# Optimization experiments

Hardware: AMD Instinct MI355X
Metric: run time of the kernel (lower is better)

The kernel has to match this reference:

```python
import jax, jax.numpy as jnp
import numpy as np

D_MODEL = 512
NUM_HEADS = 8
HEAD_DIM = D_MODEL // NUM_HEADS
WINDOW = 64


def setup_inputs() -> dict:
    key = jax.random.key(0)
    ks = jax.random.split(key, 9)
    B, S = 2, 4096
    s = 1.0 / np.sqrt(D_MODEL)
    x = jax.random.normal(ks[0], (B, S, D_MODEL), dtype=jnp.float32)
    Wq = jax.random.uniform(ks[1], (D_MODEL, D_MODEL), jnp.float32, -s, s)
    bq = jax.random.uniform(ks[2], (D_MODEL,), jnp.float32, -s, s)
    Wk = jax.random.uniform(ks[3], (D_MODEL, D_MODEL), jnp.float32, -s, s)
    bk = jax.random.uniform(ks[4], (D_MODEL,), jnp.float32, -s, s)
    Wv = jax.random.uniform(ks[5], (D_MODEL, D_MODEL), jnp.float32, -s, s)
    bv = jax.random.uniform(ks[6], (D_MODEL,), jnp.float32, -s, s)
    Wo = jax.random.uniform(ks[7], (D_MODEL, D_MODEL), jnp.float32, -s, s)
    bo = jax.random.uniform(ks[8], (D_MODEL,), jnp.float32, -s, s)
    return {"x": x, "Wq": Wq, "bq": bq, "Wk": Wk, "bk": bk,
            "Wv": Wv, "bv": bv, "Wo": Wo, "bo": bo}


def reference(x, Wq, bq, Wk, bk, Wv, bv, Wo, bo):
    B, S, _ = x.shape
    # projections (torch Linear: x @ W.T + b)
    q = (x @ Wq.T + bq).reshape(B, S, NUM_HEADS, HEAD_DIM).transpose(0, 2, 1, 3)
    k = (x @ Wk.T + bk).reshape(B, S, NUM_HEADS, HEAD_DIM).transpose(0, 2, 1, 3)
    v = (x @ Wv.T + bv).reshape(B, S, NUM_HEADS, HEAD_DIM).transpose(0, 2, 1, 3)
    scores = jnp.einsum('bhqd,bhkd->bhqk', q, k) / jnp.sqrt(
        jnp.asarray(HEAD_DIM, x.dtype))
    idx = jnp.arange(S)
    local = jnp.abs(idx[None, :] - idx[:, None]) <= WINDOW  # [S,S]
    scores = jnp.where(local[None, None], scores, -jnp.inf)
    attn = jax.nn.softmax(scores, axis=-1)
    out = jnp.einsum('bhqk,bhkd->bhqd', attn, v)
    out = out.transpose(0, 2, 1, 3).reshape(B, S, D_MODEL)
    return out @ Wo.T + bo
```

## Files before the change

kernel.cpp:

```cpp
#include <hip/hip_runtime.h>
#include <hip/hip_bf16.h>

typedef __attribute__((ext_vector_type(8))) short short8;
typedef __attribute__((ext_vector_type(4))) short s16x4;
typedef __attribute__((ext_vector_type(4))) float f32x4;

#define S_LEN 4096
#define DM 512
#define NH 8
#define HD 64
#define NB 2

__device__ __forceinline__ ushort f2bf(float f) {
    union { float f; unsigned int i; } x; x.f = f;
    unsigned int i = x.i;
    unsigned int r = (i + 0x7fffu + ((i >> 16) & 1u)) >> 16;
    return (ushort)r;
}

__device__ __forceinline__ void gload16(const ushort* g, ushort* l) {
    __builtin_amdgcn_global_load_lds(
        (const __attribute__((address_space(1))) unsigned int*)(g),
        (__attribute__((address_space(3))) unsigned int*)(l),
        16, 0, 0);
}

__device__ __forceinline__ f32x4 mfma16(s16x4 a, s16x4 b, f32x4 c) {
#if __has_builtin(__builtin_amdgcn_mfma_f32_16x16x16bf16_1k)
    return __builtin_amdgcn_mfma_f32_16x16x16bf16_1k(a, b, c, 0, 0, 0);
#else
    f32x4 d;
    asm volatile("v_mfma_f32_16x16x16_bf16 %0, %1, %2, %3"
                 : "=v"(d) : "v"(a), "v"(b), "v"(c));
    return d;
#endif
}

__global__ __launch_bounds__(256) void cvt_all_kernel(
    const float* __restrict__ x,
    const float* __restrict__ s0, const float* __restrict__ s1,
    const float* __restrict__ s2, const float* __restrict__ s3,
    ushort* __restrict__ xb,
    ushort* __restrict__ t0, ushort* __restrict__ t1,
    ushort* __restrict__ t2, ushort* __restrict__ t3)
{
    const float* src;
    ushort* dst;
    size_t i;
    if (blockIdx.x < 2048) {
        src = x; dst = xb;
        i = (size_t)blockIdx.x * 256 + threadIdx.x;
    } else {
        const int wb = blockIdx.x - 2048;
        const int which = wb >> 7;
        src = (which == 0) ? s0 : (which == 1) ? s1 : (which == 2) ? s2 : s3;
        dst = (which == 0) ? t0 : (which == 1) ? t1 : (which == 2) ? t2 : t3;
        i = (size_t)(wb & 127) * 256 + threadIdx.x;
    }
    const float4* s = (const float4*)src;
    float4 a = s[i * 2], b = s[i * 2 + 1];
    short8 o;
    o[0] = (short)f2bf(a.x); o[1] = (short)f2bf(a.y);
    o[2] = (short)f2bf(a.z); o[3] = (short)f2bf(a.w);
    o[4] = (short)f2bf(b.x); o[5] = (short)f2bf(b.y);
    o[6] = (short)f2bf(b.z); o[7] = (short)f2bf(b.w);
    *(short8*)(dst + i * 8) = o;
}

__global__ __launch_bounds__(256) void qkv_proj_kernel(
    const ushort* __restrict__ X,
    const ushort* __restrict__ Wq, const float* __restrict__ bq,
    const ushort* __restrict__ Wk, const float* __restrict__ bk,
    const ushort* __restrict__ Wv, const float* __restrict__ bv,
    ushort* __restrict__ Qws, ushort* __restrict__ Kws, ushort* __restrict__ Vt)
{
    __shared__ __align__(1024) ushort As[128 * 64];
    __shared__ __align__(1024) ushort Bs[3][64 * 64];

    const int lane = threadIdx.x & 63;
    const int w    = threadIdx.x >> 6;
    const int xcd  = blockIdx.x & 7;
    const int idx  = blockIdx.x >> 3;
    const int tc   = idx & 7;
    const int tr   = xcd + 8 * (idx >> 3);
    const int c0   = tc * 64;
    const int r0   = tr * 128;

    const ushort* Wm[3] = { Wq, Wk, Wv };
    const float*  bm[3] = { bq, bk, bv };

    const int lr = lane & 15;
    const int lg = lane >> 4;
    const int ldrow = lane >> 3;
    const int ldcol = (lane & 7) * 8;

    f32x4 acc[3][2][4] = {};
    for (int ks = 0; ks < 8; ks++) {
        const int k0 = ks * 64;
        if (ks) __syncthreads();
        const ushort* gA = X + (size_t)(r0 + ldrow) * DM + k0 + ldcol;
#pragma unroll
        for (int j = 0; j < 4; j++) {
            const int ch = w * 4 + j;
            gload16(gA + (size_t)ch * 8 * DM, As + ch * 512);
        }
#pragma unroll
        for (int j = 0; j < 6; j++) {
            const int q = w * 6 + j;
            const int mat = q >> 3, ch = q & 7;
            gload16(Wm[mat] + (size_t)(c0 + ch * 8 + ldrow) * DM + k0 + ldcol,
                    &Bs[mat][ch * 512]);
        }
        __syncthreads();

#pragma unroll
        for (int kk = 0; kk < 2; kk++) {
            const int koff = kk * 32 + lg * 8;
            short8 a[2], b[3][4];
#pragma unroll
            for (int m = 0; m < 2; m++)
                a[m] = *(const short8*)(As + (w * 32 + 16 * m + lr) * 64 + koff);
#pragma unroll
            for (int mat = 0; mat < 3; mat++)
#pragma unroll
                for (int n = 0; n < 4; n++)
                    b[mat][n] = *(const short8*)(&Bs[mat][(16 * n + lr) * 64 + koff]);
#pragma unroll
            for (int mat = 0; mat < 3; mat++)
#pragma unroll
                for (int m = 0; m < 2; m++)
#pragma unroll
                    for (int n = 0; n < 4; n++)
                        acc[mat][m][n] = __builtin_amdgcn_mfma_f32_16x16x32_bf16(
                            a[m], b[mat][n], acc[mat][m][n], 0, 0, 0);
        }
    }

#pragma unroll
    for (int mat = 0; mat < 3; mat++) {
#pragma unroll
        for (int n = 0; n < 4; n++) {
            const int c = c0 + 16 * n + lr;
            const float bb = bm[mat][c];
            const int h = c >> 6, d = c & 63;
#pragma unroll
            for (int m = 0; m < 2; m++) {
                const int row0 = r0 + w * 32 + 16 * m + 4 * lg;
                const int bidx = row0 >> 12;
                const int s0 = row0 & (S_LEN - 1);
                if (mat == 2) {
                    uint2 u;
                    u.x = (uint)f2bf(acc[2][m][n][0] + bb) |
                          ((uint)f2bf(acc[2][m][n][1] + bb) << 16);
                    u.y = (uint)f2bf(acc[2][m][n][2] + bb) |
                          ((uint)f2bf(acc[2][m][n][3] + bb) << 16);
                    *(uint2*)(Vt + ((size_t)(bidx * NH + h) * HD + d) * S_LEN + s0) = u;
                } else {
                    ushort* dst = (mat == 0) ? Qws : Kws;
#pragma unroll
                    for (int r = 0; r < 4; r++)
                        dst[((size_t)(bidx * NH + h) * S_LEN + s0 + r) * HD + d] =
                            f2bf(acc[mat][m][n][r] + bb);
                }
            }
        }
    }
}

__global__ __launch_bounds__(256) void attn_kernel(
    const ushort* __restrict__ Qws, const ushort* __restrict__ Kws,
    const ushort* __restrict__ Vt, ushort* __restrict__ AO)
{
    __shared__ __align__(1024) ushort Ks[192 * 64];
    __shared__ __align__(1024) ushort Vs[64 * 192];

    const int x   = blockIdx.x;
    const int xcd = x & 7;
    const int idx = x >> 3;
    const int bh  = xcd * 2 + (idx >> 6);
    const int qb  = idx & 63;
    const int w   = threadIdx.x >> 6;
    const int lane = threadIdx.x & 63;
    const int lr = lane & 15;
    const int lg = lane >> 4;

    const ushort* Qh = Qws + (size_t)bh * S_LEN * HD;
    const ushort* Kh = Kws + (size_t)bh * S_LEN * HD;
    const ushort* Vh = Vt  + (size_t)bh * HD * S_LEN;

    const int q0 = qb * 64 + w * 16;
    const int kstart = qb * 64 - 64;

#pragma unroll
    for (int i = 0; i < 6; i++) {
        const int sb = w * 384 + i * 64;
        const int s = sb + lane;
        const int row = s >> 3;
        const int g = (s & 7) ^ (row & 7);
        int rg = kstart + row;
        rg = (rg < 0) ? 0 : (rg >= S_LEN ? S_LEN - 1 : rg);
        gload16(Kh + (size_t)rg * HD + g * 8, Ks + sb * 8);
    }
#pragma unroll
    for (int i = 0; i < 6; i++) {
        const int sb = w * 384 + i * 64;
        const int s = sb + lane;
        const int row = s / 24;
        const int sr = s - row * 24;
        const int cr = sr ^ (row & 7);
        int cg = kstart + cr * 8;
        cg = (cg < 0) ? 0 : (cg > S_LEN - 8 ? S_LEN - 8 : cg);
        gload16(Vh + (size_t)row * S_LEN + cg, Vs + sb * 8);
    }

    short8 qa[2];
#pragma unroll
    for (int kk = 0; kk < 2; kk++)
        qa[kk] = *(const short8*)(Qh + (size_t)(q0 + lr) * HD + kk * 32 + lg * 8);

    __syncthreads();

    const int swz = (lr & 7) << 3;

    f32x4 sc[12];
#pragma unroll
    for (int ct = 0; ct < 12; ct++) {
        sc[ct] = f32x4{0.f, 0.f, 0.f, 0.f};
        const int base = (ct * 16 + lr) * 64;
        short8 kb0 = *(const short8*)(Ks + (base + ((0  + lg * 8) ^ swz)));
        short8 kb1 = *(const short8*)(Ks + (base + ((32 + lg * 8) ^ swz)));
        sc[ct] = __builtin_amdgcn_mfma_f32_16x16x32_bf16(kb0, qa[0], sc[ct], 0, 0, 0);
        sc[ct] = __builtin_amdgcn_mfma_f32_16x16x32_bf16(kb1, qa[1], sc[ct], 0, 0, 0);
    }

    const float scale2 = 0.18033688f;
    const int qi = q0 + lr;
    float sum = 0.f;
#pragma unroll
    for (int ct = 0; ct < 12; ct++) {
#pragma unroll
        for (int r = 0; r < 4; r++) {
            const int j = kstart + ct * 16 + 4 * lg + r;
            const bool valid = (j >= 0) && (j < S_LEN) && (qi - j <= 64) && (j - qi <= 64);
            const float p = valid ? exp2f(sc[ct][r] * scale2) : 0.f;
            sc[ct][r] = p;
            sum += p;
        }
    }
    sum += __shfl_xor(sum, 16);
    sum += __shfl_xor(sum, 32);
    const float inv = 1.0f / sum;

    s16x4 pb[12];
#pragma unroll
    for (int ct = 0; ct < 12; ct++) {
        pb[ct][0] = (short)f2bf(sc[ct][0]);
        pb[ct][1] = (short)f2bf(sc[ct][1]);
        pb[ct][2] = (short)f2bf(sc[ct][2]);
        pb[ct][3] = (short)f2bf(sc[ct][3]);
    }

    f32x4 po[4] = {};
#pragma unroll
    for (int ct = 0; ct < 12; ct++) {
        const int k0 = ct * 16 + 4 * lg;
        const int sub = k0 & 7;
        const int ch = k0 >> 3;
#pragma unroll
        for (int n = 0; n < 4; n++) {
            const int d = 16 * n + lr;
            s16x4 va = *(const s16x4*)(Vs + d * 192 + 8 * (ch ^ (lr & 7)) + sub);
            po[n] = mfma16(va, pb[ct], po[n]);
        }
    }

    const int b = bh >> 3, h = bh & 7;
    ushort* aorow = AO + ((size_t)(b * S_LEN + q0 + lr)) * DM + h * HD;
#pragma unroll
    for (int n = 0; n < 4; n++) {
        uint2 u;
        u.x = (uint)f2bf(po[n][0] * inv) | ((uint)f2bf(po[n][1] * inv) << 16);
        u.y = (uint)f2bf(po[n][2] * inv) | ((uint)f2bf(po[n][3] * inv) << 16);
        *(uint2*)(aorow + 16 * n + 4 * lg) = u;
    }
}

__global__ __launch_bounds__(256) void out_proj_kernel(
    const ushort* __restrict__ AO, const ushort* __restrict__ Wo,
    const float* __restrict__ bo, float* __restrict__ Out)
{
    __shared__ __align__(1024) ushort As[64 * 64];
    __shared__ __align__(1024) ushort Bs[128 * 64];

    const int lane = threadIdx.x & 63;
    const int w    = threadIdx.x >> 6;
    const int xcd  = blockIdx.x & 7;
    const int idx  = blockIdx.x >> 3;
    const int tr   = xcd + 8 * (idx >> 2);
    const int tc   = idx & 3;
    const int c0   = tc * 128;
    const int r0   = tr * 64;
    const int lr = lane & 15;
    const int lg = lane >> 4;
    const int wr = w >> 1, wc = w & 1;
    const int ldrow = lane >> 3;
    const int ldcol = (lane & 7) * 8;

    f32x4 acc[2][4] = {};
    for (int ks = 0; ks < 8; ks++) {
        const int k0 = ks * 64;
        if (ks) __syncthreads();
        const ushort* gA = AO + (size_t)(r0 + ldrow) * DM + k0 + ldcol;
        const ushort* gB = Wo + (size_t)(c0 + ldrow) * DM + k0 + ldcol;
#pragma unroll
        for (int j = 0; j < 2; j++) {
            const int ch = w * 2 + j;
            gload16(gA + (size_t)ch * 8 * DM, As + ch * 512);
        }
#pragma unroll
        for (int j = 0; j < 4; j++) {
            const int ch = w * 4 + j;
            gload16(gB + (size_t)ch * 8 * DM, Bs + ch * 512);
        }
        __syncthreads();

#pragma unroll
        for (int kk = 0; kk < 2; kk++) {
            const int koff = kk * 32 + lg * 8;
            short8 a[2], b[4];
#pragma unroll
            for (int m = 0; m < 2; m++)
                a[m] = *(const short8*)(As + (wr * 32 + 16 * m + lr) * 64 + koff);
#pragma unroll
            for (int n = 0; n < 4; n++)
                b[n] = *(const short8*)(Bs + (wc * 64 + 16 * n + lr) * 64 + koff);
#pragma unroll
            for (int m = 0; m < 2; m++)
#pragma unroll
                for (int n = 0; n < 4; n++)
                    acc[m][n] = __builtin_amdgcn_mfma_f32_16x16x32_bf16(a[m], b[n], acc[m][n], 0, 0, 0);
        }
    }

#pragma unroll
    for (int n = 0; n < 4; n++) {
        const int c = c0 + wc * 64 + 16 * n + lr;
        const float bb = bo[c];
#pragma unroll
        for (int m = 0; m < 2; m++) {
#pragma unroll
            for (int r = 0; r < 4; r++) {
                const int row = r0 + wr * 32 + 16 * m + 4 * lg + r;
                Out[(size_t)row * DM + c] = acc[m][n][r] + bb;
            }
        }
    }
}

extern "C" void kernel_launch(void* const* d_in, const int* in_sizes, int n_in,
                              void* d_out, int out_size, void* d_ws, size_t ws_size,
                              hipStream_t stream) {
    const float* x  = (const float*)d_in[0];
    const float* Wq = (const float*)d_in[1];
    const float* bq = (const float*)d_in[2];
    const float* Wk = (const float*)d_in[3];
    const float* bk = (const float*)d_in[4];
    const float* Wv = (const float*)d_in[5];
    const float* bv = (const float*)d_in[6];
    const float* Wo = (const float*)d_in[7];
    const float* bo = (const float*)d_in[8];
    float* out = (float*)d_out;

    const size_t XE = (size_t)NB * S_LEN * DM;
    const size_t WE = (size_t)DM * DM;

    ushort* Xb  = (ushort*)d_ws;
    ushort* Wqb = Xb + XE;
    ushort* Wkb = Wqb + WE;
    ushort* Wvb = Wkb + WE;
    ushort* Wob = Wvb + WE;
    ushort* Qws = Wob + WE;
    ushort* Kws = Qws + XE;
    ushort* Vt  = Kws + XE;
    ushort* AO  = Vt + XE;

    cvt_all_kernel<<<2560, 256, 0, stream>>>(x, Wq, Wk, Wv, Wo, Xb, Wqb, Wkb, Wvb, Wob);
    qkv_proj_kernel<<<512, 256, 0, stream>>>(Xb, Wqb, bq, Wkb, bk, Wvb, bv, Qws, Kws, Vt);
    attn_kernel<<<1024, 256, 0, stream>>>(Qws, Kws, Vt, AO);
    out_proj_kernel<<<512, 256, 0, stream>>>(AO, Wob, bo, out);
}
```

Before: 58.29 us.

## Fuse all four stages into one persistent cooperative kernel with grid syncs

Adds a persistent cooperative kernel that runs conversion, QKV projection, windowed attention and output projection in sequence, separated by grid-wide syncs and using grid-stride loops over virtual blocks. It is launched through hipLaunchCooperativeKernel when supported, capped at 512 blocks, and falls back to the four separate launches otherwise. The aim is to remove per-kernel launch overhead and inter-kernel gaps. In exchange it accepts grid.sync costs, a smaller grid than the separate kernels used, and extra host-side attribute and occupancy queries on every call.

```diff
diff --git a/kernel.cpp b/kernel.cpp
--- a/kernel.cpp
+++ b/kernel.cpp
@@ -1,5 +1,8 @@
 #include <hip/hip_runtime.h>
 #include <hip/hip_bf16.h>
+#include <hip/hip_cooperative_groups.h>
+
+namespace cg = cooperative_groups;
 
 typedef __attribute__((ext_vector_type(8))) short short8;
 typedef __attribute__((ext_vector_type(4))) short s16x4;
@@ -34,6 +37,317 @@
                  : "=v"(d) : "v"(a), "v"(b), "v"(c));
     return d;
 #endif
+}
+
+__global__ __launch_bounds__(256) void fused_kernel(
+    const float* __restrict__ x,
+    const float* __restrict__ Wq, const float* __restrict__ bq,
+    const float* __restrict__ Wk, const float* __restrict__ bk,
+    const float* __restrict__ Wv, const float* __restrict__ bv,
+    const float* __restrict__ Wo, const float* __restrict__ bo,
+    float* __restrict__ Out,
+    ushort* __restrict__ Xb, ushort* __restrict__ Wqb, ushort* __restrict__ Wkb,
+    ushort* __restrict__ Wvb, ushort* __restrict__ Wob,
+    ushort* __restrict__ Qws, ushort* __restrict__ Kws,
+    ushort* __restrict__ Vtp, ushort* __restrict__ AO)
+{
+    __shared__ __align__(1024) ushort lds[16384];
+
+    cg::grid_group grid = cg::this_grid();
+
+    const int lane = threadIdx.x & 63;
+    const int w    = threadIdx.x >> 6;
+    const int lr = lane & 15;
+    const int lg = lane >> 4;
+    const int ldrow = lane >> 3;
+    const int ldcol = (lane & 7) * 8;
+
+    {
+        const int stride = gridDim.x * 256;
+        const int tid = blockIdx.x * 256 + threadIdx.x;
+        for (int t = tid; t < 655360; t += stride) {
+            const float* src; ushort* dst; size_t i;
+            if (t < 524288) { src = x; dst = Xb; i = (size_t)t; }
+            else {
+                const int wt = t - 524288;
+                const int which = wt >> 15;
+                i = (size_t)(wt & 32767);
+                src = (which == 0) ? Wq : (which == 1) ? Wk : (which == 2) ? Wv : Wo;
+                dst = (which == 0) ? Wqb : (which == 1) ? Wkb : (which == 2) ? Wvb : Wob;
+            }
+            const float4* s = (const float4*)src;
+            float4 a = s[i * 2], b = s[i * 2 + 1];
+            short8 o;
+            o[0] = (short)f2bf(a.x); o[1] = (short)f2bf(a.y);
+            o[2] = (short)f2bf(a.z); o[3] = (short)f2bf(a.w);
+            o[4] = (short)f2bf(b.x); o[5] = (short)f2bf(b.y);
+            o[6] = (short)f2bf(b.z); o[7] = (short)f2bf(b.w);
+            *(short8*)(dst + i * 8) = o;
+        }
+    }
+    grid.sync();
+
+    {
+        ushort* As  = lds;
+        ushort* Bsp = lds + 4096;
+        const ushort* Wm[3] = { Wqb, Wkb, Wvb };
+        const float*  bm[3] = { bq, bk, bv };
+
+        for (int vb = blockIdx.x; vb < 1024; vb += gridDim.x) {
+            __syncthreads();
+            const int xcd = vb & 7;
+            const int idx = vb >> 3;
+            const int tc  = idx & 7;
+            const int tr  = xcd + 8 * (idx >> 3);
+            const int c0  = tc * 64;
+            const int r0  = tr * 64;
+
+            f32x4 acc[3][4] = {};
+            for (int ks = 0; ks < 8; ks++) {
+                const int k0 = ks * 64;
+                if (ks) __syncthreads();
+                const ushort* gA = Xb + (size_t)(r0 + ldrow) * DM + k0 + ldcol;
+#pragma unroll
+                for (int j = 0; j < 2; j++) {
+                    const int ch = w * 2 + j;
+                    gload16(gA + (size_t)ch * 8 * DM, As + ch * 512);
+                }
+#pragma unroll
+                for (int j = 0; j < 6; j++) {
+                    const int q = w * 6 + j;
+                    const int mat = q >> 3, ch = q & 7;
+                    gload16(Wm[mat] + (size_t)(c0 + ch * 8 + ldrow) * DM + k0 + ldcol,
+                            Bsp + mat * 4096 + ch * 512);
+                }
+                __syncthreads();
+
+#pragma unroll
+                for (int kk = 0; kk < 2; kk++) {
+                    const int koff = kk * 32 + lg * 8;
+                    short8 a = *(const short8*)(As + (w * 16 + lr) * 64 + koff);
+#pragma unroll
+                    for (int mat = 0; mat < 3; mat++)
+#pragma unroll
+                        for (int n = 0; n < 4; n++) {
+                            short8 b = *(const short8*)(Bsp + mat * 4096 + (16 * n + lr) * 64 + koff);
+                            acc[mat][n] = __builtin_amdgcn_mfma_f32_16x16x32_bf16(
+                                a, b, acc[mat][n], 0, 0, 0);
+                        }
+                }
+            }
+
+#pragma unroll
+            for (int mat = 0; mat < 3; mat++) {
+#pragma unroll
+                for (int n = 0; n < 4; n++) {
+                    const int c = c0 + 16 * n + lr;
+                    const float bb = bm[mat][c];
+                    const int h = c >> 6, d = c & 63;
+                    const int row0 = r0 + w * 16 + 4 * lg;
+                    const int bidx = row0 >> 12;
+                    const int s0 = row0 & (S_LEN - 1);
+                    if (mat == 2) {
+                        uint2 u;
+                        u.x = (uint)f2bf(acc[2][n][0] + bb) |
+                              ((uint)f2bf(acc[2][n][1] + bb) << 16);
+                        u.y = (uint)f2bf(acc[2][n][2] + bb) |
+                              ((uint)f2bf(acc[2][n][3] + bb) << 16);
+                        *(uint2*)(Vtp + ((size_t)(bidx * NH + h) * HD + d) * S_LEN + s0) = u;
+                    } else {
+                        ushort* dst = (mat == 0) ? Qws : Kws;
+#pragma unroll
+                        for (int r = 0; r < 4; r++)
+                            dst[((size_t)(bidx * NH + h) * S_LEN + s0 + r) * HD + d] =
+                                f2bf(acc[mat][n][r] + bb);
+                    }
+                }
+            }
+        }
+    }
+    grid.sync();
+
+    {
+        ushort* KVs = lds;
+
+        for (int vb = blockIdx.x; vb < 1024; vb += gridDim.x) {
+            __syncthreads();
+            const int xcd = vb & 7;
+            const int idx = vb >> 3;
+            const int bh  = xcd * 2 + (idx >> 6);
+            const int qb  = idx & 63;
+
+            const ushort* Qh = Qws + (size_t)bh * S_LEN * HD;
+            const ushort* Kh = Kws + (size_t)bh * S_LEN * HD;
+            const ushort* Vh = Vtp + (size_t)bh * HD * S_LEN;
+
+            const int q0 = qb * 64 + w * 16;
+            const int kstart = qb * 64 - 64;
+
+#pragma unroll
+            for (int i = 0; i < 6; i++) {
+                const int sb = w * 384 + i * 64;
+                const int s = sb + lane;
+                const int row = s >> 3;
+                const int g = (s & 7) ^ (row & 7);
+                int rg = kstart + row;
+                rg = (rg < 0) ? 0 : (rg >= S_LEN ? S_LEN - 1 : rg);
+                gload16(Kh + (size_t)rg * HD + g * 8, KVs + sb * 8);
+            }
+            short8 qa[2];
+#pragma unroll
+            for (int kk = 0; kk < 2; kk++)
+                qa[kk] = *(const short8*)(Qh + (size_t)(q0 + lr) * HD + kk * 32 + lg * 8);
+
+            __syncthreads();
+
+            const int swz = (lr & 7) << 3;
+
+            f32x4 sc[12];
+#pragma unroll
+            for (int ct = 0; ct < 12; ct++) {
+                sc[ct] = f32x4{0.f, 0.f, 0.f, 0.f};
+                const int base = (ct * 16 + lr) * 64;
+                short8 kb0 = *(const short8*)(KVs + (base + ((0  + lg * 8) ^ swz)));
+                short8 kb1 = *(const short8*)(KVs + (base + ((32 + lg * 8) ^ swz)));
+                sc[ct] = __builtin_amdgcn_mfma_f32_16x16x32_bf16(kb0, qa[0], sc[ct], 0, 0, 0);
+                sc[ct] = __builtin_amdgcn_mfma_f32_16x16x32_bf16(kb1, qa[1], sc[ct], 0, 0, 0);
+            }
+
+            __syncthreads();
+
+#pragma unroll
+            for (int i = 0; i < 6; i++) {
+                const int sb = w * 384 + i * 64;
+                const int s = sb + lane;
+                const int row = s / 24;
+                const int sr = s - row * 24;
+                const int cr = sr ^ (row & 7);
+                int cg = kstart + cr * 8;
+                cg = (cg < 0) ? 0 : (cg > S_LEN - 8 ? S_LEN - 8 : cg);
+                gload16(Vh + (size_t)row * S_LEN + cg, KVs + sb * 8);
+            }
+
+            const float scale2 = 0.18033688f;
+            const int qi = q0 + lr;
+            float sum = 0.f;
+#pragma unroll
+            for (int ct = 0; ct < 12; ct++) {
+#pragma unroll
+                for (int r = 0; r < 4; r++) {
+                    const int j = kstart + ct * 16 + 4 * lg + r;
+                    const bool valid = (j >= 0) && (j < S_LEN) && (qi - j <= 64) && (j - qi <= 64);
+                    const float p = valid ? exp2f(sc[ct][r] * scale2) : 0.f;
+                    sc[ct][r] = p;
+                    sum += p;
+                }
+            }
+            sum += __shfl_xor(sum, 16);
+            sum += __shfl_xor(sum, 32);
+            const float inv = 1.0f / sum;
+
+            s16x4 pb[12];
+#pragma unroll
+            for (int ct = 0; ct < 12; ct++) {
+                pb[ct][0] = (short)f2bf(sc[ct][0]);
+                pb[ct][1] = (short)f2bf(sc[ct][1]);
+                pb[ct][2] = (short)f2bf(sc[ct][2]);
+                pb[ct][3] = (short)f2bf(sc[ct][3]);
+            }
+
+            __syncthreads();
+
+            f32x4 po[4] = {};
+#pragma unroll
+            for (int ct = 0; ct < 12; ct++) {
+                const int k0 = ct * 16 + 4 * lg;
+                const int sub = k0 & 7;
+                const int ch = k0 >> 3;
+#pragma unroll
+                for (int n = 0; n < 4; n++) {
+                    const int d = 16 * n + lr;
+                    s16x4 va = *(const s16x4*)(KVs + d * 192 + 8 * (ch ^ (lr & 7)) + sub);
+                    po[n] = mfma16(va, pb[ct], po[n]);
+                }
+            }
+
+            const int b = bh >> 3, h = bh & 7;
+            ushort* aorow = AO + ((size_t)(b * S_LEN + q0 + lr)) * DM + h * HD;
+#pragma unroll
+            for (int n = 0; n < 4; n++) {
+                uint2 u;
+                u.x = (uint)f2bf(po[n][0] * inv) | ((uint)f2bf(po[n][1] * inv) << 16);
+                u.y = (uint)f2bf(po[n][2] * inv) | ((uint)f2bf(po[n][3] * inv) << 16);
+                *(uint2*)(aorow + 16 * n + 4 * lg) = u;
+            }
+        }
+    }
+    grid.sync();
+
+    {
+        ushort* As = lds;
+        ushort* Bs = lds + 4096;
+
+        for (int vb = blockIdx.x; vb < 512; vb += gridDim.x) {
+            __syncthreads();
+            const int xcd = vb & 7;
+            const int idx = vb >> 3;
+            const int tr  = xcd + 8 * (idx >> 2);
+            const int tc  = idx & 3;
+            const int c0  = tc * 128;
+            const int r0  = tr * 64;
+            const int wr = w >> 1, wc = w & 1;
+
+            f32x4 acc[2][4] = {};
+            for (int ks = 0; ks < 8; ks++) {
+                const int k0 = ks * 64;
+                if (ks) __syncthreads();
+                const ushort* gA = AO + (size_t)(r0 + ldrow) * DM + k0 + ldcol;
+                const ushort* gB = Wob + (size_t)(c0 + ldrow) * DM + k0 + ldcol;
+#pragma unroll
+                for (int j = 0; j < 2; j++) {
+                    const int ch = w * 2 + j;
+                    gload16(gA + (size_t)ch * 8 * DM, As + ch * 512);
+                }
+#pragma unroll
+                for (int j = 0; j < 4; j++) {
+                    const int ch = w * 4 + j;
+                    gload16(gB + (size_t)ch * 8 * DM, Bs + ch * 512);
+                }
+                __syncthreads();
+
+#pragma unroll
+                for (int kk = 0; kk < 2; kk++) {
+                    const int koff = kk * 32 + lg * 8;
+                    short8 a[2], b[4];
+#pragma unroll
+                    for (int m = 0; m < 2; m++)
+                        a[m] = *(const short8*)(As + (wr * 32 + 16 * m + lr) * 64 + koff);
+#pragma unroll
+                    for (int n = 0; n < 4; n++)
+                        b[n] = *(const short8*)(Bs + (wc * 64 + 16 * n + lr) * 64 + koff);
+#pragma unroll
+                    for (int m = 0; m < 2; m++)
+#pragma unroll
+                        for (int n = 0; n < 4; n++)
+                            acc[m][n] = __builtin_amdgcn_mfma_f32_16x16x32_bf16(a[m], b[n], acc[m][n], 0, 0, 0);
+                }
+            }
+
+#pragma unroll
+            for (int n = 0; n < 4; n++) {
+                const int c = c0 + wc * 64 + 16 * n + lr;
+                const float bb = bo[c];
+#pragma unroll
+                for (int m = 0; m < 2; m++) {
+#pragma unroll
+                    for (int r = 0; r < 4; r++) {
+                        const int row = r0 + wr * 32 + 16 * m + 4 * lg + r;
+                        Out[(size_t)row * DM + c] = acc[m][n][r] + bb;
+                    }
+                }
+            }
+        }
+    }
 }
 
 __global__ __launch_bounds__(256) void cvt_all_kernel(
@@ -384,6 +698,34 @@
     ushort* Vt  = Kws + XE;
     ushort* AO  = Vt + XE;
 
+    int dev = 0;
+    hipGetDevice(&dev);
+    int coop = 0;
+    hipDeviceGetAttribute(&coop, hipDeviceAttributeCooperativeLaunch, dev);
+    int nCU = 0;
+    hipDeviceGetAttribute(&nCU, hipDeviceAttributeMultiprocessorCount, dev);
+    int maxBlk = 0;
+    hipOccupancyMaxActiveBlocksPerMultiprocessor(&maxBlk, (const void*)fused_kernel, 256, 0);
+
+    if (coop && maxBlk >= 1 && nCU >= 8) {
+        int grid = maxBlk * nCU;
+        if (grid > 512) grid = 512;
+        const float *xa = x, *wqa = Wq, *bqa = bq, *wka = Wk, *bka = bk,
+                    *wva = Wv, *bva = bv, *woa = Wo, *boa = bo;
+        float* outa = out;
+        ushort *Xba = Xb, *Wqba = Wqb, *Wkba = Wkb, *Wvba = Wvb, *Woba = Wob,
+               *Qwsa = Qws, *Kwsa = Kws, *Vta = Vt, *AOa = AO;
+        void* args[] = {
+            (void*)&xa, (void*)&wqa, (void*)&bqa, (void*)&wka, (void*)&bka,
+            (void*)&wva, (void*)&bva, (void*)&woa, (void*)&boa, (void*)&outa,
+            (void*)&Xba, (void*)&Wqba, (void*)&Wkba, (void*)&Wvba, (void*)&Woba,
+            (void*)&Qwsa, (void*)&Kwsa, (void*)&Vta, (void*)&AOa
+        };
+        hipError_t err = hipLaunchCooperativeKernel(
+            (const void*)fused_kernel, dim3(grid), dim3(256), args, 0, stream);
+        if (err == hipSuccess) return;
+    }
+
     cvt_all_kernel<<<2560, 256, 0, stream>>>(x, Wq, Wk, Wv, Wo, Xb, Wqb, Wkb, Wvb, Wob);
     qkv_proj_kernel<<<512, 256, 0, stream>>>(Xb, Wqb, bq, Wkb, bk, Wvb, bv, Qws, Kws, Vt);
     attn_kernel<<<1024, 256, 0, stream>>>(Qws, Kws, Vt, AO);
```

Result: slower. 196.5 us (+237.0%).

## Process two query blocks per attention workgroup to share K/V tiles

Applied to the files above, without the earlier changes.

Each attention workgroup now handles two consecutive 64-row query blocks, loading a 256-row K/V window once instead of two overlapping 192-row windows, and the grid is halved. V loads are issued after the first barrier so they overlap with the first block's QK^T and softmax, with a second barrier before P·V. This cuts redundant global loads of K/V but doubles LDS per block and halves the number of workgroups, which may reduce occupancy and latency hiding.

```diff
diff --git a/kernel.cpp b/kernel.cpp
--- a/kernel.cpp
+++ b/kernel.cpp
@@ -171,14 +171,15 @@
     const ushort* __restrict__ Qws, const ushort* __restrict__ Kws,
     const ushort* __restrict__ Vt, ushort* __restrict__ AO)
 {
-    __shared__ __align__(1024) ushort Ks[192 * 64];
-    __shared__ __align__(1024) ushort Vs[64 * 192];
+    __shared__ __align__(1024) ushort Ks[256 * 64];
+    __shared__ __align__(1024) ushort Vs[64 * 256];
 
     const int x   = blockIdx.x;
     const int xcd = x & 7;
     const int idx = x >> 3;
-    const int bh  = xcd * 2 + (idx >> 6);
-    const int qb  = idx & 63;
+    const int bh  = xcd * 2 + (idx >> 5);
+    const int qg  = idx & 31;
+    const int qb0 = qg * 2;
     const int w   = threadIdx.x >> 6;
     const int lane = threadIdx.x & 63;
     const int lr = lane & 15;
@@ -188,12 +189,11 @@
     const ushort* Kh = Kws + (size_t)bh * S_LEN * HD;
     const ushort* Vh = Vt  + (size_t)bh * HD * S_LEN;
 
-    const int q0 = qb * 64 + w * 16;
-    const int kstart = qb * 64 - 64;
-
-#pragma unroll
-    for (int i = 0; i < 6; i++) {
-        const int sb = w * 384 + i * 64;
+    const int kstart = qb0 * 64 - 64;
+
+#pragma unroll
+    for (int i = 0; i < 8; i++) {
+        const int sb = w * 512 + i * 64;
         const int s = sb + lane;
         const int row = s >> 3;
         const int g = (s & 7) ^ (row & 7);
@@ -201,87 +201,99 @@
         rg = (rg < 0) ? 0 : (rg >= S_LEN ? S_LEN - 1 : rg);
         gload16(Kh + (size_t)rg * HD + g * 8, Ks + sb * 8);
     }
-#pragma unroll
-    for (int i = 0; i < 6; i++) {
-        const int sb = w * 384 + i * 64;
+
+    short8 qa[2][2];
+#pragma unroll
+    for (int p = 0; p < 2; p++)
+#pragma unroll
+        for (int kk = 0; kk < 2; kk++)
+            qa[p][kk] = *(const short8*)(
+                Qh + (size_t)(qb0 * 64 + p * 64 + w * 16 + lr) * HD + kk * 32 + lg * 8);
+
+    __syncthreads();
+
+#pragma unroll
+    for (int i = 0; i < 8; i++) {
+        const int sb = w * 512 + i * 64;
         const int s = sb + lane;
-        const int row = s / 24;
-        const int sr = s - row * 24;
+        const int row = s >> 5;
+        const int sr = s & 31;
         const int cr = sr ^ (row & 7);
         int cg = kstart + cr * 8;
         cg = (cg < 0) ? 0 : (cg > S_LEN - 8 ? S_LEN - 8 : cg);
         gload16(Vh + (size_t)row * S_LEN + cg, Vs + sb * 8);
     }
 
-    short8 qa[2];
-#pragma unroll
-    for (int kk = 0; kk < 2; kk++)
-        qa[kk] = *(const short8*)(Qh + (size_t)(q0 + lr) * HD + kk * 32 + lg * 8);
-
-    __syncthreads();
-
     const int swz = (lr & 7) << 3;
-
-    f32x4 sc[12];
-#pragma unroll
-    for (int ct = 0; ct < 12; ct++) {
-        sc[ct] = f32x4{0.f, 0.f, 0.f, 0.f};
-        const int base = (ct * 16 + lr) * 64;
-        short8 kb0 = *(const short8*)(Ks + (base + ((0  + lg * 8) ^ swz)));
-        short8 kb1 = *(const short8*)(Ks + (base + ((32 + lg * 8) ^ swz)));
-        sc[ct] = __builtin_amdgcn_mfma_f32_16x16x32_bf16(kb0, qa[0], sc[ct], 0, 0, 0);
-        sc[ct] = __builtin_amdgcn_mfma_f32_16x16x32_bf16(kb1, qa[1], sc[ct], 0, 0, 0);
-    }
-
     const float scale2 = 0.18033688f;
-    const int qi = q0 + lr;
-    float sum = 0.f;
-#pragma unroll
-    for (int ct = 0; ct < 12; ct++) {
-#pragma unroll
-        for (int r = 0; r < 4; r++) {
-            const int j = kstart + ct * 16 + 4 * lg + r;
-            const bool valid = (j >= 0) && (j < S_LEN) && (qi - j <= 64) && (j - qi <= 64);
-            const float p = valid ? exp2f(sc[ct][r] * scale2) : 0.f;
-            sc[ct][r] = p;
-            sum += p;
-        }
-    }
-    sum += __shfl_xor(sum, 16);
-    sum += __shfl_xor(sum, 32);
-    const float inv = 1.0f / sum;
-
-    s16x4 pb[12];
-#pragma unroll
-    for (int ct = 0; ct < 12; ct++) {
-        pb[ct][0] = (short)f2bf(sc[ct][0]);
-        pb[ct][1] = (short)f2bf(sc[ct][1]);
-        pb[ct][2] = (short)f2bf(sc[ct][2]);
-        pb[ct][3] = (short)f2bf(sc[ct][3]);
-    }
-
-    f32x4 po[4] = {};
-#pragma unroll
-    for (int ct = 0; ct < 12; ct++) {
-        const int k0 = ct * 16 + 4 * lg;
-        const int sub = k0 & 7;
-        const int ch = k0 >> 3;
+
+#pragma unroll
+    for (int p = 0; p < 2; p++) {
+        const int poff = p * 64;
+        const int q0 = qb0 * 64 + poff + w * 16;
+
+        f32x4 sc[12];
+#pragma unroll
+        for (int ct = 0; ct < 12; ct++) {
+            sc[ct] = f32x4{0.f, 0.f, 0.f, 0.f};
+            const int base = (poff + ct * 16 + lr) * 64;
+            short8 kb0 = *(const short8*)(Ks + (base + ((0  + lg * 8) ^ swz)));
+            short8 kb1 = *(const short8*)(Ks + (base + ((32 + lg * 8) ^ swz)));
+            sc[ct] = __builtin_amdgcn_mfma_f32_16x16x32_bf16(kb0, qa[p][0], sc[ct], 0, 0, 0);
+            sc[ct] = __builtin_amdgcn_mfma_f32_16x16x32_bf16(kb1, qa[p][1], sc[ct], 0, 0, 0);
+        }
+
+        const int qi = q0 + lr;
+        float sum = 0.f;
+#pragma unroll
+        for (int ct = 0; ct < 12; ct++) {
+#pragma unroll
+            for (int r = 0; r < 4; r++) {
+                const int j = kstart + poff + ct * 16 + 4 * lg + r;
+                const bool valid = (j >= 0) && (j < S_LEN) && (qi - j <= 64) && (j - qi <= 64);
+                const float pp = valid ? exp2f(sc[ct][r] * scale2) : 0.f;
+                sc[ct][r] = pp;
+                sum += pp;
+            }
+        }
+        sum += __shfl_xor(sum, 16);
+        sum += __shfl_xor(sum, 32);
+        const float inv = 1.0f / sum;
+
+        s16x4 pb[12];
+#pragma unroll
+        for (int ct = 0; ct < 12; ct++) {
+            pb[ct][0] = (short)f2bf(sc[ct][0]);
+            pb[ct][1] = (short)f2bf(sc[ct][1]);
+            pb[ct][2] = (short)f2bf(sc[ct][2]);
+            pb[ct][3] = (short)f2bf(sc[ct][3]);
+        }
+
+        if (p == 0) __syncthreads();
+
+        f32x4 po[4] = {};
+#pragma unroll
+        for (int ct = 0; ct < 12; ct++) {
+            const int k0 = poff + ct * 16 + 4 * lg;
+            const int sub = k0 & 7;
+            const int ch = k0 >> 3;
+#pragma unroll
+            for (int n = 0; n < 4; n++) {
+                const int d = 16 * n + lr;
+                s16x4 va = *(const s16x4*)(Vs + d * 256 + 8 * (ch ^ (lr & 7)) + sub);
+                po[n] = mfma16(va, pb[ct], po[n]);
+            }
+        }
+
+        const int b = bh >> 3, h = bh & 7;
+        ushort* aorow = AO + ((size_t)(b * S_LEN + q0 + lr)) * DM + h * HD;
 #pragma unroll
         for (int n = 0; n < 4; n++) {
-            const int d = 16 * n + lr;
-            s16x4 va = *(const s16x4*)(Vs + d * 192 + 8 * (ch ^ (lr & 7)) + sub);
-            po[n] = mfma16(va, pb[ct], po[n]);
-        }
-    }
-
-    const int b = bh >> 3, h = bh & 7;
-    ushort* aorow = AO + ((size_t)(b * S_LEN + q0 + lr)) * DM + h * HD;
-#pragma unroll
-    for (int n = 0; n < 4; n++) {
-        uint2 u;
-        u.x = (uint)f2bf(po[n][0] * inv) | ((uint)f2bf(po[n][1] * inv) << 16);
-        u.y = (uint)f2bf(po[n][2] * inv) | ((uint)f2bf(po[n][3] * inv) << 16);
-        *(uint2*)(aorow + 16 * n + 4 * lg) = u;
+            uint2 u;
+            u.x = (uint)f2bf(po[n][0] * inv) | ((uint)f2bf(po[n][1] * inv) << 16);
+            u.y = (uint)f2bf(po[n][2] * inv) | ((uint)f2bf(po[n][3] * inv) << 16);
+            *(uint2*)(aorow + 16 * n + 4 * lg) = u;
+        }
     }
 }
 
@@ -386,6 +398,6 @@
 
     cvt_all_kernel<<<2560, 256, 0, stream>>>(x, Wq, Wk, Wv, Wo, Xb, Wqb, Wkb, Wvb, Wob);
     qkv_proj_kernel<<<512, 256, 0, stream>>>(Xb, Wqb, bq, Wkb, bk, Wvb, bv, Qws, Kws, Vt);
-    attn_kernel<<<1024, 256, 0, stream>>>(Qws, Kws, Vt, AO);
+    attn_kernel<<<512, 256, 0, stream>>>(Qws, Kws, Vt, AO);
     out_proj_kernel<<<512, 256, 0, stream>>>(AO, Wob, bo, out);
 }
```

Result: slower. 62.60 us (+7.4%).
